# Optimization experiments

Measured on AMD Instinct MI355X. Metric: run time of the kernel, lower is better.

Reference implementation:

```python
import jax, jax.numpy as jnp
import numpy as np

B, L, D, H = 2, 2048, 1024, 16
DH = D // H


def setup_inputs() -> dict:
    key = jax.random.key(0)
    ks = jax.random.split(key, 12)
    s = 0.02
    return {
        "q": jax.random.normal(ks[0], (B, L, D), jnp.float32),
        "k": jax.random.normal(ks[1], (B, L, D), jnp.float32),
        "v": jax.random.normal(ks[2], (B, L, D), jnp.float32),
        "pos_enc": jax.random.normal(ks[3], (L + 1, D), jnp.float32),
        "Wq": jax.random.normal(ks[4], (D, D), jnp.float32) * s,
        "bq": jnp.zeros((D,), jnp.float32),
        "Wk": jax.random.normal(ks[5], (D, D), jnp.float32) * s,
        "bk": jnp.zeros((D,), jnp.float32),
        "Wv": jax.random.normal(ks[6], (D, D), jnp.float32) * s,
        "bv": jnp.zeros((D,), jnp.float32),
        "Wo": jax.random.normal(ks[7], (D, D), jnp.float32) * s,
        "bo": jnp.zeros((D,), jnp.float32),
        "r_w_bias": jax.random.normal(ks[8], (H, 1, DH), jnp.float32) * s,
        "r_r_bias": jax.random.normal(ks[9], (H, 1, DH), jnp.float32) * s,
        "r_kernel": jax.random.normal(ks[10], (H, D, DH), jnp.float32) * s,
    }


def reference(q, k, v, pos_enc, Wq, bq, Wk, bk, Wv, bv, Wo, bo,
              r_w_bias, r_r_bias, r_kernel):
    b, lq, d = q.shape
    h, _, dh = r_w_bias.shape
    lk = k.shape[1]
    scale = dh ** -0.5

    # q/k/v projections, then split heads: [b, l, d] -> [b, h, l, dh]
    qh = (q @ Wq + bq).reshape(b, lq, h, dh).transpose(0, 2, 1, 3)
    kh = (k @ Wk + bk).reshape(b, lk, h, dh).transpose(0, 2, 1, 3)
    vh = (v @ Wv + bv).reshape(b, lk, h, dh).transpose(0, 2, 1, 3)

    # content scores with global content bias (Transformer-XL r_w_bias)
    scores = jnp.einsum('bhqd,bhkd->bhqk', qh + r_w_bias, kh) * scale

    # relative-position term: pos_enc [p, d] @ r_kernel [h, d, dh] -> [h, p, dh]
    pe = jnp.einsum('pd,hde->hpe', pos_enc, r_kernel)
    rel = jnp.einsum('bhqd,hpd->bhqp', qh + r_r_bias, pe) * scale  # [b,h,lq,p]
    p = rel.shape[-1]
    shift = 1 + (lq != lk)
    # rel-shift trick: reshape with swapped last two dims, drop first `shift`
    # rows, reshape back, keep first lk columns
    rel = rel.reshape(b, h, p, lq)[:, :, shift:, :]
    rel = rel.reshape(b, h, lq, p - shift)[..., :lk]
    scores = scores + rel

    # causal mask (key_cache is None path): subtract 1e7 on strict upper triangle
    causal_mask = jnp.triu(jnp.ones((lq, lk), dtype=bool), 1)
    scores = scores - causal_mask * 1e7

    out = jnp.einsum('bhqk,bhkd->bhqd', jax.nn.softmax(scores, axis=-1), vh)
    out = out.transpose(0, 2, 1, 3).reshape(b, lq, d)  # merge heads
    return out @ Wo + bo
```

## Files before the change

### kernel.cpp

```cpp
#include <hip/hip_runtime.h>
#include <hip/hip_bf16.h>

typedef __attribute__((ext_vector_type(8))) short bf16x8;
typedef __attribute__((ext_vector_type(4))) float f32x4;
typedef __attribute__((ext_vector_type(16))) float f32x16;
typedef unsigned short u16;
typedef unsigned int u32;

#define DEV static __device__ __forceinline__

DEV u16 f2us(float x) {
  __hip_bfloat16 h = __float2bfloat16(x);
  union { __hip_bfloat16 h; u16 u; } c; c.h = h; return c.u;
}
DEV float us2f(u16 u) {
  union { __hip_bfloat16 h; u16 u; } c; c.u = u;
  return __bfloat162float(c.h);
}
DEV f32x16 mfma32(bf16x8 a, bf16x8 b, f32x16 c) {
  return __builtin_amdgcn_mfma_f32_32x32x16_bf16(a, b, c, 0, 0, 0);
}
DEV u32 pkbf(float a, float b) {
  return (u32)f2us(a) | ((u32)f2us(b) << 16);
}
DEV void gl16(const u16* g, u16* l) {
  __builtin_amdgcn_global_load_lds(
      (const __attribute__((address_space(1))) unsigned int*)(g),
      (__attribute__((address_space(3))) unsigned int*)(l), 16, 0, 0);
}

constexpr int PE_ROWS = 2144;
constexpr int PE_M    = 2176;
constexpr float QSCALE = 0.125f;

constexpr size_t SZ_QKV  = (size_t)4096 * 1024 * 2;
constexpr size_t SZ_W    = (size_t)1024 * 1024 * 2;
constexpr size_t SZ_POSB = (size_t)PE_M * 1024 * 2;
constexpr size_t OFF_QB   = 0;
constexpr size_t OFF_KB   = OFF_QB  + SZ_QKV;
constexpr size_t OFF_VB   = OFF_KB  + SZ_QKV;
constexpr size_t OFF_WQT  = OFF_VB  + SZ_QKV;
constexpr size_t OFF_WKT  = OFF_WQT + SZ_W;
constexpr size_t OFF_WVT  = OFF_WKT + SZ_W;
constexpr size_t OFF_WOT  = OFF_WVT + SZ_W;
constexpr size_t OFF_RKT  = OFF_WOT + SZ_W;
constexpr size_t OFF_POSB = OFF_RKT + SZ_W;
constexpr size_t OFF_QW   = OFF_POSB + SZ_POSB;
constexpr size_t OFF_QR   = OFF_QW  + SZ_QKV;
constexpr size_t OFF_KH   = OFF_QR  + SZ_QKV;
constexpr size_t OFF_VT   = OFF_KH  + SZ_QKV;
constexpr size_t OFF_PEH  = OFF_VT  + SZ_QKV;
constexpr size_t OFF_ATTNB = OFF_QB;

struct PrepPtrs {
  const float4 *q, *k, *v, *pos;
  u16 *qb, *kb, *vb, *posb;
  const float *Wq, *Wk, *Wv, *Wo, *rk;
  u16 *Wqt, *Wkt, *Wvt, *Wot, *Rkt;
};

__global__ __launch_bounds__(256)
void k_prep(PrepPtrs P)
{
  __shared__ float t[32][33];
  const int bid = blockIdx.x;
  if (bid < 14464) {
    const float4* src; u16* dst; int i, n4in, n4tot;
    if (bid < 4096)       { src = P.q;   dst = P.qb;   i = bid * 256 + threadIdx.x;           n4in = 1048576; n4tot = 1048576; }
    else if (bid < 8192)  { src = P.k;   dst = P.kb;   i = (bid - 4096) * 256 + threadIdx.x;  n4in = 1048576; n4tot = 1048576; }
    else if (bid < 12288) { src = P.v;   dst = P.vb;   i = (bid - 8192) * 256 + threadIdx.x;  n4in = 1048576; n4tot = 1048576; }
    else                  { src = P.pos; dst = P.posb; i = (bid - 12288) * 256 + threadIdx.x; n4in = 524544;  n4tot = 557056; }
    if (i >= n4tot) return;
    float4 val;
    if (i < n4in) val = src[i];
    else { val.x = val.y = val.z = val.w = 0.f; }
    ushort4 o;
    o.x = f2us(val.x); o.y = f2us(val.y); o.z = f2us(val.z); o.w = f2us(val.w);
    *reinterpret_cast<ushort4*>(dst + (size_t)i * 4) = o;
    return;
  }
  const int tx = threadIdx.x & 31, ty = threadIdx.x >> 5;
  if (bid < 18560) {
    const int tt = bid - 14464;
    const int z = tt >> 10, rr = tt & 1023;
    const float* in = (z == 0) ? P.Wq : (z == 1) ? P.Wk : (z == 2) ? P.Wv : P.Wo;
    u16* out = (z == 0) ? P.Wqt : (z == 1) ? P.Wkt : (z == 2) ? P.Wvt : P.Wot;
    const int kb0 = (rr & 31) * 32, nb0 = (rr >> 5) * 32;
#pragma unroll
    for (int r = 0; r < 32; r += 8)
      t[ty + r][tx] = in[(size_t)(kb0 + ty + r) * 1024 + nb0 + tx];
    __syncthreads();
#pragma unroll
    for (int r = 0; r < 32; r += 8)
      out[(size_t)(nb0 + ty + r) * 1024 + kb0 + tx] = f2us(t[tx][ty + r]);
    return;
  }
  {
    const int tt = bid - 18560;
    const int e = tt & 1, d = (tt >> 1) & 31, h = tt >> 6;
    const int eb0 = e * 32, db0 = d * 32;
#pragma unroll
    for (int r = 0; r < 32; r += 8)
      t[ty + r][tx] = P.rk[(size_t)h * 65536 + (size_t)(db0 + ty + r) * 64 + eb0 + tx];
    __syncthreads();
#pragma unroll
    for (int r = 0; r < 32; r += 8)
      P.Rkt[(size_t)(h * 64 + eb0 + ty + r) * 1024 + db0 + tx] = f2us(t[tx][ty + r]);
  }
}

struct ProjPtrs {
  const u16 *A0, *A1, *A2, *A3;
  const u16 *B0, *B1, *B2, *B3;
  const float *bias0, *bias1, *bias2;
  const float *rwb, *rrb;
  u16 *Qw, *Qr, *Kh, *Vt, *PEh;
};

__global__ __launch_bounds__(256)
void k_gemm_proj(ProjPtrs pp)
{
  const int z = blockIdx.z;
  if (z == 3 && blockIdx.y >= PE_M / 128) return;
  const u16* A  = (z == 0) ? pp.A0 : (z == 1) ? pp.A1 : (z == 2) ? pp.A2 : pp.A3;
  const u16* Bt = (z == 0) ? pp.B0 : (z == 1) ? pp.B1 : (z == 2) ? pp.B2 : pp.B3;

  __shared__ __attribute__((aligned(16))) u16 As[128 * 32];
  __shared__ __attribute__((aligned(16))) u16 Bs[128 * 32];
  const int tid  = threadIdx.x;
  const int lane = tid & 63;
  const int wave = tid >> 6;
  const int bm = blockIdx.y * 128;
  const int bn = blockIdx.x * 128;
  const int wr = (wave >> 1) * 64;
  const int wc = (wave & 1) * 64;
  const int fr = lane & 15;
  const int fk = (lane >> 4) * 8;

  f32x4 zero = {0.f, 0.f, 0.f, 0.f};
  f32x4 acc[4][4];
#pragma unroll
  for (int m = 0; m < 4; ++m)
#pragma unroll
    for (int n = 0; n < 4; ++n) acc[m][n] = zero;

  const int cA = wave * 2;
  const u16* gA = A  + (size_t)(bm + cA * 16 + (lane >> 2)) * 1024 + (lane & 3) * 8;
  const u16* gB = Bt + (size_t)(bn + cA * 16 + (lane >> 2)) * 1024 + (lane & 3) * 8;
  u16* lA = As + cA * 512;
  u16* lB = Bs + cA * 512;

  for (int k0 = 0; k0 < 1024; k0 += 32) {
    gl16(gA + k0, lA);
    gl16(gA + 16 * 1024 + k0, lA + 512);
    gl16(gB + k0, lB);
    gl16(gB + 16 * 1024 + k0, lB + 512);
    __syncthreads();
    bf16x8 af[4], bfv[4];
#pragma unroll
    for (int m = 0; m < 4; ++m) af[m]  = *(const bf16x8*)(&As[(wr + m * 16 + fr) * 32 + fk]);
#pragma unroll
    for (int n = 0; n < 4; ++n) bfv[n] = *(const bf16x8*)(&Bs[(wc + n * 16 + fr) * 32 + fk]);
#pragma unroll
    for (int m = 0; m < 4; ++m)
#pragma unroll
      for (int n = 0; n < 4; ++n)
        acc[m][n] = __builtin_amdgcn_mfma_f32_16x16x32_bf16(af[m], bfv[n], acc[m][n], 0, 0, 0);
    __syncthreads();
  }

#pragma unroll
  for (int m = 0; m < 4; ++m)
#pragma unroll
    for (int n = 0; n < 4; ++n)
#pragma unroll
      for (int r = 0; r < 4; ++r) {
        const int grow = bm + wr + m * 16 + (lane >> 4) * 4 + r;
        const int gcol = bn + wc + n * 16 + fr;
        float v = acc[m][n][r];
        const int b_ = grow >> 11, l_ = grow & 2047;
        const int h_ = gcol >> 6,  e_ = gcol & 63;
        if (z == 0) {
          v += pp.bias0[gcol];
          const size_t o = (((size_t)(b_ * 16 + h_) * 2048 + l_) << 6) + e_;
          pp.Qw[o] = f2us((v + pp.rwb[gcol]) * QSCALE);
          pp.Qr[o] = f2us((v + pp.rrb[gcol]) * QSCALE);
        } else if (z == 1) {
          v += pp.bias1[gcol];
          const size_t o = (((size_t)(b_ * 16 + h_) * 2048 + l_) << 6) + e_;
          pp.Kh[o] = f2us(v);
        } else if (z == 2) {
          v += pp.bias2[gcol];
          const size_t o = (((size_t)(b_ * 16 + h_) * 64 + e_) << 11) + l_;
          pp.Vt[o] = f2us(v);
        } else {
          if (grow < PE_ROWS) {
            const size_t o = ((size_t)h_ * PE_ROWS + grow) * 64 + e_;
            pp.PEh[o] = f2us(v);
          }
        }
      }
}

__global__ __launch_bounds__(256)
void k_gemm_o(const u16* __restrict__ A, const u16* __restrict__ Bt,
              const float* __restrict__ bias, float* __restrict__ outf)
{
  __shared__ __attribute__((aligned(16))) u16 As[128 * 32];
  __shared__ __attribute__((aligned(16))) u16 Bs[128 * 32];
  const int tid  = threadIdx.x;
  const int lane = tid & 63;
  const int wave = tid >> 6;
  const int bm = blockIdx.y * 128;
  const int bn = blockIdx.x * 128;
  const int wr = (wave >> 1) * 64;
  const int wc = (wave & 1) * 64;
  const int fr = lane & 15;
  const int fk = (lane >> 4) * 8;

  f32x4 zero = {0.f, 0.f, 0.f, 0.f};
  f32x4 acc[4][4];
#pragma unroll
  for (int m = 0; m < 4; ++m)
#pragma unroll
    for (int n = 0; n < 4; ++n) acc[m][n] = zero;

  const int cA = wave * 2;
  const u16* gA = A  + (size_t)(bm + cA * 16 + (lane >> 2)) * 1024 + (lane & 3) * 8;
  const u16* gB = Bt + (size_t)(bn + cA * 16 + (lane >> 2)) * 1024 + (lane & 3) * 8;
  u16* lA = As + cA * 512;
  u16* lB = Bs + cA * 512;

  for (int k0 = 0; k0 < 1024; k0 += 32) {
    gl16(gA + k0, lA);
    gl16(gA + 16 * 1024 + k0, lA + 512);
    gl16(gB + k0, lB);
    gl16(gB + 16 * 1024 + k0, lB + 512);
    __syncthreads();
    bf16x8 af[4], bfv[4];
#pragma unroll
    for (int m = 0; m < 4; ++m) af[m]  = *(const bf16x8*)(&As[(wr + m * 16 + fr) * 32 + fk]);
#pragma unroll
    for (int n = 0; n < 4; ++n) bfv[n] = *(const bf16x8*)(&Bs[(wc + n * 16 + fr) * 32 + fk]);
#pragma unroll
    for (int m = 0; m < 4; ++m)
#pragma unroll
      for (int n = 0; n < 4; ++n)
        acc[m][n] = __builtin_amdgcn_mfma_f32_16x16x32_bf16(af[m], bfv[n], acc[m][n], 0, 0, 0);
    __syncthreads();
  }

#pragma unroll
  for (int m = 0; m < 4; ++m)
#pragma unroll
    for (int n = 0; n < 4; ++n)
#pragma unroll
      for (int r = 0; r < 4; ++r) {
        const int grow = bm + wr + m * 16 + (lane >> 4) * 4 + r;
        const int gcol = bn + wc + n * 16 + fr;
        outf[(size_t)grow * 1024 + gcol] = acc[m][n][r] + bias[gcol];
      }
}


#define PV_HALF(WARR)                                                          \
  {                                                                            \
    _Pragma("unroll")                                                          \
    for (int kvs = 0; kvs < 2; ++kvs) {                                        \
      u32 snd0 = hi ? WARR[4 * kvs]     : WARR[4 * kvs + 2];                   \
      u32 snd1 = hi ? WARR[4 * kvs + 1] : WARR[4 * kvs + 3];                   \
      u32 r0 = (u32)__shfl_xor((int)snd0, 32);                                 \
      u32 r1 = (u32)__shfl_xor((int)snd1, 32);                                 \
      union { u32 u[4]; bf16x8 v; } pf;                                        \
      pf.u[0] = hi ? r0 : WARR[4 * kvs];                                       \
      pf.u[1] = hi ? r1 : WARR[4 * kvs + 1];                                   \
      pf.u[2] = hi ? WARR[4 * kvs + 2] : r0;                                   \
      pf.u[3] = hi ? WARR[4 * kvs + 3] : r1;                                   \
      bf16x8 v0_ = *(const bf16x8*)(V_h + (size_t)l31 * 2048 + c0h_            \
                                    + kvs * 16 + hi * 8);                      \
      bf16x8 v1_ = *(const bf16x8*)(V_h + (size_t)(32 + l31) * 2048 + c0h_     \
                                    + kvs * 16 + hi * 8);                      \
      Oc0 = mfma32(v0_, pf.v, Oc0);                                            \
      Oc1 = mfma32(v1_, pf.v, Oc1);                                            \
    }                                                                          \
  }

#define ATTN_HALF(q0v, c0_, KT)                                                \
  {                                                                            \
    const int c0h_ = (c0_) + (KT) * 32;                                        \
    f32x16 sv_ = {};                                                           \
    {                                                                          \
      bf16x8 qwf_[4], kf_[4];                                                  \
      _Pragma("unroll")                                                        \
      for (int kk = 0; kk < 4; ++kk) {                                         \
        qwf_[kk] = *(const bf16x8*)(Qw_h + (size_t)((q0v) + l31) * 64          \
                                    + kk * 16 + hi * 8);                       \
        kf_[kk] = *(const bf16x8*)(K_h + (size_t)(c0h_ + l31) * 64 + kk * 16   \
                                   + hi * 8);                                  \
      }                                                                        \
      _Pragma("unroll")                                                        \
      for (int kk = 0; kk < 4; ++kk) sv_ = mfma32(kf_[kk], qwf_[kk], sv_);     \
    }                                                                          \
    _Pragma("unroll")                                                          \
    for (int r = 0; r < 16; ++r) {                                             \
      const int pat = (r & 3) + 8 * (r >> 2) + 4 * hi;                         \
      float x = sv_[r] + us2f(Ew[l31][(KT) * 32 + pat + 31 - l31]);            \
      if (c0h_ + pat > (q0v) + l31) x = -1e30f;                                \
      sv_[r] = x;                                                              \
    }                                                                          \
    float mx_ = sv_[0];                                                        \
    _Pragma("unroll")                                                          \
    for (int r = 1; r < 16; ++r) mx_ = fmaxf(mx_, sv_[r]);                     \
    mx_ = fmaxf(mx_, __shfl_xor(mx_, 32));                                     \
    const float mn_ = fmaxf(mrun, mx_);                                        \
    const float al_ = __expf(mrun - mn_);                                      \
    mrun = mn_;                                                                \
    float rsum_ = 0.f;                                                         \
    u32 wa_[8];                                                                \
    _Pragma("unroll")                                                          \
    for (int g8 = 0; g8 < 8; ++g8) {                                           \
      float pa_ = __expf(sv_[2 * g8] - mn_);                                   \
      float pb_ = __expf(sv_[2 * g8 + 1] - mn_);                               \
      u16 ua_ = f2us(pa_), ub_ = f2us(pb_);                                    \
      rsum_ += us2f(ua_) + us2f(ub_);                                          \
      wa_[g8] = (u32)ua_ | ((u32)ub_ << 16);                                   \
    }                                                                          \
    ls = ls * al_ + rsum_ + __shfl_xor(rsum_, 32);                             \
    Oc0 *= al_;                                                                \
    Oc1 *= al_;                                                                \
    PV_HALF(wa_)                                                               \
  }

#define ATTN_STEP(q0v, stv)                                                    \
  {                                                                            \
    const int c0_ = (stv) * 64;                                                \
    const int Jb_ = 2048 + c0_ - (q0v) - 31;                                   \
    {                                                                          \
      bf16x8 qrf_[4];                                                          \
      _Pragma("unroll")                                                        \
      for (int kk = 0; kk < 4; ++kk)                                           \
        qrf_[kk] = *(const bf16x8*)(Qr_h + (size_t)((q0v) + l31) * 64          \
                                    + kk * 16 + hi * 8);                       \
      _Pragma("unroll")                                                        \
      for (int tau = 0; tau < 3; ++tau) {                                      \
        f32x16 e_ = {};                                                        \
        {                                                                      \
          bf16x8 pe_[4];                                                       \
          _Pragma("unroll")                                                    \
          for (int kk = 0; kk < 4; ++kk)                                       \
            pe_[kk] = *(const bf16x8*)(PE_h + (size_t)(Jb_ + tau * 32 + l31)   \
                                       * 64 + kk * 16 + hi * 8);               \
          _Pragma("unroll")                                                    \
          for (int kk = 0; kk < 4; ++kk) e_ = mfma32(pe_[kk], qrf_[kk], e_);   \
        }                                                                      \
        _Pragma("unroll")                                                      \
        for (int g4 = 0; g4 < 4; ++g4) {                                       \
          uint2 w2_;                                                           \
          w2_.x = pkbf(e_[4 * g4 + 0], e_[4 * g4 + 1]);                        \
          w2_.y = pkbf(e_[4 * g4 + 2], e_[4 * g4 + 3]);                        \
          *(uint2*)(&Ew[l31][tau * 32 + 8 * g4 + 4 * hi]) = w2_;               \
        }                                                                      \
      }                                                                        \
    }                                                                          \
    ATTN_HALF(q0v, c0_, 0)                                                     \
    ATTN_HALF(q0v, c0_, 1)                                                     \
  }

#define OBROUND(PRE, SCL)                                                      \
  {                                                                            \
    _Pragma("unroll")                                                          \
    for (int g4 = 0; g4 < 4; ++g4) {                                           \
      float* pb0 = &Obuf[l31][8 * g4 + 4 * hi];                                \
      float* pb1 = &Obuf[l31][32 + 8 * g4 + 4 * hi];                           \
      float2 a0 = *(float2*)pb0,       a1 = *(float2*)(pb0 + 2);               \
      float2 b0 = *(float2*)pb1,       b1 = *(float2*)(pb1 + 2);               \
      a0.x = a0.x * (PRE) + Oc0[4 * g4 + 0] * (SCL);                           \
      a0.y = a0.y * (PRE) + Oc0[4 * g4 + 1] * (SCL);                           \
      a1.x = a1.x * (PRE) + Oc0[4 * g4 + 2] * (SCL);                           \
      a1.y = a1.y * (PRE) + Oc0[4 * g4 + 3] * (SCL);                           \
      b0.x = b0.x * (PRE) + Oc1[4 * g4 + 0] * (SCL);                           \
      b0.y = b0.y * (PRE) + Oc1[4 * g4 + 1] * (SCL);                           \
      b1.x = b1.x * (PRE) + Oc1[4 * g4 + 2] * (SCL);                           \
      b1.y = b1.y * (PRE) + Oc1[4 * g4 + 3] * (SCL);                           \
      *(float2*)pb0 = a0; *(float2*)(pb0 + 2) = a1;                            \
      *(float2*)pb1 = b0; *(float2*)(pb1 + 2) = b1;                            \
    }                                                                          \
  }

__global__ __launch_bounds__(256, 4)
void k_attn(const u16* __restrict__ Qw, const u16* __restrict__ Qr,
            const u16* __restrict__ Kh, const u16* __restrict__ Vt,
            const u16* __restrict__ PEh, u16* __restrict__ attnb)
{
  const int bid = blockIdx.x;
  const int xcd = bid & 7, s = bid >> 3;
  const int p = s & 31, g = s >> 5;
  const int hb = xcd + 8 * g;
  const int h = hb & 15, b = hb >> 4;
  const int wave = threadIdx.x >> 6, lane = threadIdx.x & 63;
  const int l31 = lane & 31, hi = lane >> 5;

  const int qtL = 63 - p, qtS = p;
  const int q0L = qtL * 32, q0S = qtS * 32;
  const int nstL = qtL / 2 + 1;

  const u16* Qw_h = Qw + (size_t)hb * (2048 * 64);
  const u16* Qr_h = Qr + (size_t)hb * (2048 * 64);
  const u16* K_h  = Kh + (size_t)hb * (2048 * 64);
  const u16* V_h  = Vt + (size_t)hb * (64 * 2048);
  const u16* PE_h = PEh + (size_t)h * (PE_ROWS * 64);

  __shared__ __attribute__((aligned(16))) u16 Elds_all[4][32][100];
  __shared__ float Obuf[32][66];
  __shared__ float mlb[2][4][2][32];
  u16 (*Ew)[100] = Elds_all[wave];

  const int lo  = wave ? 9 + 8 * (wave - 1) : 0;
  const int hiE = lo + (wave ? 8 : 9);
  const int la0 = lo;
  const int la1 = hiE < nstL ? hiE : nstL;
  const int lb0 = lo > nstL ? lo : nstL;
  const int lb1 = hiE;
  const bool hasL = la1 > la0;
  const bool hasS = lb1 > lb0;
  const bool crossing = hasL && hasS;

  const f32x16 vzero = {};
  f32x16 Oc0 = {}, Oc1 = {};
  float mrun = -1e30f, ls = 0.f;

  if (hasL) {
    for (int st = la0; st < la1; ++st) ATTN_STEP(q0L, st)
  }
  if (crossing) {
    OBROUND(0.f, 1.f)
    if (hi == 0) { mlb[0][wave][0][l31] = mrun; mlb[0][wave][1][l31] = ls; }
    Oc0 = vzero; Oc1 = vzero; mrun = -1e30f; ls = 0.f;
  }
  if (hasS) {
    for (int st = lb0 - nstL; st < lb1 - nstL; ++st) ATTN_STEP(q0S, st)
  }

  if (hi == 0) {
    if (crossing) {
      mlb[1][wave][0][l31] = mrun; mlb[1][wave][1][l31] = ls;
    } else if (hasL) {
      mlb[0][wave][0][l31] = mrun;  mlb[0][wave][1][l31] = ls;
      mlb[1][wave][0][l31] = -1e30f; mlb[1][wave][1][l31] = 0.f;
    } else {
      mlb[1][wave][0][l31] = mrun;  mlb[1][wave][1][l31] = ls;
      mlb[0][wave][0][l31] = -1e30f; mlb[0][wave][1][l31] = 0.f;
    }
  }
  __syncthreads();

  const bool cwExists = (nstL != 17) && (nstL != 25);
  const int  cw = (nstL < 25) ? 2 : 3;

  const float mstL = fmaxf(fmaxf(mlb[0][0][0][l31], mlb[0][1][0][l31]),
                           fmaxf(mlb[0][2][0][l31], mlb[0][3][0][l31]));
  if (wave == 0) {
    const float preL = cwExists ? __expf(mlb[0][cw][0][l31] - mstL) : 0.f;
    const float scl = __expf(mrun - mstL);
    OBROUND(preL, scl)
  }
  __syncthreads();
  if (wave == 1) {
    const float scl = __expf(mrun - mstL);
    OBROUND(1.f, scl)
  }
  __syncthreads();
  if (wave == 2 && hasL && !crossing) {
    const float scl = __expf(mrun - mstL);
    OBROUND(1.f, scl)
  }
  __syncthreads();
  if (wave == 0) {
    float lst = 0.f;
#pragma unroll
    for (int w = 0; w < 4; ++w)
      lst += mlb[0][w][1][l31] * __expf(mlb[0][w][0][l31] - mstL);
    const float inv = 1.f / lst;
    const size_t orow = ((size_t)(b * 2048 + q0L + l31)) * 1024 + h * 64 + hi * 32;
#pragma unroll
    for (int j4 = 0; j4 < 32; j4 += 4) {
      float2 t0 = *(float2*)&Obuf[l31][hi * 32 + j4];
      float2 t1 = *(float2*)&Obuf[l31][hi * 32 + j4 + 2];
      ushort4 st;
      st.x = f2us(t0.x * inv); st.y = f2us(t0.y * inv);
      st.z = f2us(t1.x * inv); st.w = f2us(t1.y * inv);
      *(ushort4*)(attnb + orow + j4) = st;
    }
  }
  __syncthreads();

  const float mstS = fmaxf(mlb[1][2][0][l31], mlb[1][3][0][l31]);
  if (wave == 2 && hasS) {
    const float scl = __expf(mrun - mstS);
    OBROUND(0.f, scl)
  }
  __syncthreads();
  if (wave == 3) {
    const float scl = __expf(mrun - mstS);
    const float pre = (nstL < 25) ? 1.f : 0.f;
    OBROUND(pre, scl)
  }
  __syncthreads();
  if (wave == 1) {
    float lst = mlb[1][2][1][l31] * __expf(mlb[1][2][0][l31] - mstS)
              + mlb[1][3][1][l31] * __expf(mlb[1][3][0][l31] - mstS);
    const float inv = 1.f / lst;
    const size_t orow = ((size_t)(b * 2048 + q0S + l31)) * 1024 + h * 64 + hi * 32;
#pragma unroll
    for (int j4 = 0; j4 < 32; j4 += 4) {
      float2 t0 = *(float2*)&Obuf[l31][hi * 32 + j4];
      float2 t1 = *(float2*)&Obuf[l31][hi * 32 + j4 + 2];
      ushort4 st;
      st.x = f2us(t0.x * inv); st.y = f2us(t0.y * inv);
      st.z = f2us(t1.x * inv); st.w = f2us(t1.y * inv);
      *(ushort4*)(attnb + orow + j4) = st;
    }
  }
}

extern "C" void kernel_launch(void* const* d_in, const int* in_sizes, int n_in,
                              void* d_out, int out_size, void* d_ws, size_t ws_size,
                              hipStream_t stream)
{
  const float* q   = (const float*)d_in[0];
  const float* k   = (const float*)d_in[1];
  const float* v   = (const float*)d_in[2];
  const float* pos = (const float*)d_in[3];
  const float* Wq  = (const float*)d_in[4];
  const float* bq  = (const float*)d_in[5];
  const float* Wk  = (const float*)d_in[6];
  const float* bk  = (const float*)d_in[7];
  const float* Wv  = (const float*)d_in[8];
  const float* bv  = (const float*)d_in[9];
  const float* Wo  = (const float*)d_in[10];
  const float* bo  = (const float*)d_in[11];
  const float* rwb = (const float*)d_in[12];
  const float* rrb = (const float*)d_in[13];
  const float* rk  = (const float*)d_in[14];

  char* ws = (char*)d_ws;
  u16* qb    = (u16*)(ws + OFF_QB);
  u16* kb    = (u16*)(ws + OFF_KB);
  u16* vb    = (u16*)(ws + OFF_VB);
  u16* Wqt   = (u16*)(ws + OFF_WQT);
  u16* Wkt   = (u16*)(ws + OFF_WKT);
  u16* Wvt   = (u16*)(ws + OFF_WVT);
  u16* Wot   = (u16*)(ws + OFF_WOT);
  u16* Rkt   = (u16*)(ws + OFF_RKT);
  u16* posb  = (u16*)(ws + OFF_POSB);
  u16* Qw    = (u16*)(ws + OFF_QW);
  u16* Qr    = (u16*)(ws + OFF_QR);
  u16* Kh    = (u16*)(ws + OFF_KH);
  u16* Vt    = (u16*)(ws + OFF_VT);
  u16* PEh   = (u16*)(ws + OFF_PEH);
  u16* attnb = (u16*)(ws + OFF_ATTNB);
  float* outf = (float*)d_out;

  PrepPtrs P;
  P.q = (const float4*)q; P.k = (const float4*)k; P.v = (const float4*)v;
  P.pos = (const float4*)pos;
  P.qb = qb; P.kb = kb; P.vb = vb; P.posb = posb;
  P.Wq = Wq; P.Wk = Wk; P.Wv = Wv; P.Wo = Wo; P.rk = rk;
  P.Wqt = Wqt; P.Wkt = Wkt; P.Wvt = Wvt; P.Wot = Wot; P.Rkt = Rkt;
  k_prep<<<dim3(19584), 256, 0, stream>>>(P);

  ProjPtrs pp;
  pp.A0 = qb;  pp.A1 = kb;  pp.A2 = vb;  pp.A3 = posb;
  pp.B0 = Wqt; pp.B1 = Wkt; pp.B2 = Wvt; pp.B3 = Rkt;
  pp.bias0 = bq; pp.bias1 = bk; pp.bias2 = bv;
  pp.rwb = rwb; pp.rrb = rrb;
  pp.Qw = Qw; pp.Qr = Qr; pp.Kh = Kh; pp.Vt = Vt; pp.PEh = PEh;
  k_gemm_proj<<<dim3(8, 32, 4), 256, 0, stream>>>(pp);

  k_attn<<<dim3(1024), 256, 0, stream>>>(Qw, Qr, Kh, Vt, PEh, attnb);

  k_gemm_o<<<dim3(8, 32), 256, 0, stream>>>(attnb, Wot, bo, outf);
}
```

Measured before the change: 243.4 us.

## Share double-buffered K/V LDS tiles across four per-wave query tiles in attention

The attention kernel is restructured so each block handles four 32-row query tiles (one per wave, paired short/long for causal balance) over a shared key sweep. K and V tiles are staged into swizzled, double-buffered LDS, replacing per-wave direct global loads. The previous split-KV work sharing across waves, with its LDS merge and multiple barriers, is removed. Grid halves to 512 blocks and launch bounds drop to 2 blocks/SM, trading occupancy and per-step barriers (waves finishing early still sync) for K/V reuse.

Result: slower. 268.2 us (+10.2%).

```diff
diff --git a/kernel.cpp b/kernel.cpp
--- a/kernel.cpp
+++ b/kernel.cpp
@@ -263,7 +263,22 @@
 }
 
 
-#define PV_HALF(WARR)                                                          \
+#define STAGE(STV, BB)                                                         \
+  {                                                                            \
+    const int c0s_ = (STV) * 64;                                               \
+    _Pragma("unroll")                                                          \
+    for (int cc = 0; cc < 2; ++cc) {                                           \
+      const int Pu = cc * 256 + wave * 64 + lane;                              \
+      const int ru = Pu >> 3;                                                  \
+      const int cbu = (Pu & 7) ^ (ru & 7);                                     \
+      gl16(K_h + (size_t)(c0s_ + ru) * 64 + cbu * 8,                           \
+           &KS[BB][(cc * 256 + wave * 64) * 8]);                               \
+      gl16(V_h + (size_t)ru * 2048 + c0s_ + cbu * 8,                           \
+           &VS[BB][(cc * 256 + wave * 64) * 8]);                               \
+    }                                                                          \
+  }
+
+#define PV_HALF(WARR, KT, BB)                                                  \
   {                                                                            \
     _Pragma("unroll")                                                          \
     for (int kvs = 0; kvs < 2; ++kvs) {                                        \
@@ -276,27 +291,27 @@
       pf.u[1] = hi ? r1 : WARR[4 * kvs + 1];                                   \
       pf.u[2] = hi ? WARR[4 * kvs + 2] : r0;                                   \
       pf.u[3] = hi ? WARR[4 * kvs + 3] : r1;                                   \
-      bf16x8 v0_ = *(const bf16x8*)(V_h + (size_t)l31 * 2048 + c0h_            \
-                                    + kvs * 16 + hi * 8);                      \
-      bf16x8 v1_ = *(const bf16x8*)(V_h + (size_t)(32 + l31) * 2048 + c0h_     \
-                                    + kvs * 16 + hi * 8);                      \
+      const int cbv_ = ((KT) * 4 + kvs * 2 + hi) ^ (l31 & 7);                  \
+      bf16x8 v0_ = *(const bf16x8*)(&VS[BB][l31 * 64 + cbv_ * 8]);             \
+      bf16x8 v1_ = *(const bf16x8*)(&VS[BB][(32 + l31) * 64 + cbv_ * 8]);      \
       Oc0 = mfma32(v0_, pf.v, Oc0);                                            \
       Oc1 = mfma32(v1_, pf.v, Oc1);                                            \
     }                                                                          \
   }
 
-#define ATTN_HALF(q0v, c0_, KT)                                                \
+#define ATTN_HALF(c0_, KT, BB)                                                 \
   {                                                                            \
     const int c0h_ = (c0_) + (KT) * 32;                                        \
     f32x16 sv_ = {};                                                           \
     {                                                                          \
+      const int rk_ = (KT) * 32 + l31;                                         \
       bf16x8 qwf_[4], kf_[4];                                                  \
       _Pragma("unroll")                                                        \
       for (int kk = 0; kk < 4; ++kk) {                                         \
-        qwf_[kk] = *(const bf16x8*)(Qw_h + (size_t)((q0v) + l31) * 64          \
+        qwf_[kk] = *(const bf16x8*)(Qw_h + (size_t)(q0 + l31) * 64             \
                                     + kk * 16 + hi * 8);                       \
-        kf_[kk] = *(const bf16x8*)(K_h + (size_t)(c0h_ + l31) * 64 + kk * 16   \
-                                   + hi * 8);                                  \
+        const int cbk_ = (kk * 2 + hi) ^ (rk_ & 7);                            \
+        kf_[kk] = *(const bf16x8*)(&KS[BB][rk_ * 64 + cbk_ * 8]);              \
       }                                                                        \
       _Pragma("unroll")                                                        \
       for (int kk = 0; kk < 4; ++kk) sv_ = mfma32(kf_[kk], qwf_[kk], sv_);     \
@@ -305,7 +320,7 @@
     for (int r = 0; r < 16; ++r) {                                             \
       const int pat = (r & 3) + 8 * (r >> 2) + 4 * hi;                         \
       float x = sv_[r] + us2f(Ew[l31][(KT) * 32 + pat + 31 - l31]);            \
-      if (c0h_ + pat > (q0v) + l31) x = -1e30f;                                \
+      if (c0h_ + pat > q0 + l31) x = -1e30f;                                   \
       sv_[r] = x;                                                              \
     }                                                                          \
     float mx_ = sv_[0];                                                        \
@@ -328,18 +343,18 @@
     ls = ls * al_ + rsum_ + __shfl_xor(rsum_, 32);                             \
     Oc0 *= al_;                                                                \
     Oc1 *= al_;                                                                \
-    PV_HALF(wa_)                                                               \
-  }
-
-#define ATTN_STEP(q0v, stv)                                                    \
+    PV_HALF(wa_, KT, BB)                                                       \
+  }
+
+#define ATTN_STEP(stv, BB)                                                     \
   {                                                                            \
     const int c0_ = (stv) * 64;                                                \
-    const int Jb_ = 2048 + c0_ - (q0v) - 31;                                   \
+    const int Jb_ = 2048 + c0_ - q0 - 31;                                      \
     {                                                                          \
       bf16x8 qrf_[4];                                                          \
       _Pragma("unroll")                                                        \
       for (int kk = 0; kk < 4; ++kk)                                           \
-        qrf_[kk] = *(const bf16x8*)(Qr_h + (size_t)((q0v) + l31) * 64          \
+        qrf_[kk] = *(const bf16x8*)(Qr_h + (size_t)(q0 + l31) * 64             \
                                     + kk * 16 + hi * 8);                       \
       _Pragma("unroll")                                                        \
       for (int tau = 0; tau < 3; ++tau) {                                      \
@@ -362,47 +377,28 @@
         }                                                                      \
       }                                                                        \
     }                                                                          \
-    ATTN_HALF(q0v, c0_, 0)                                                     \
-    ATTN_HALF(q0v, c0_, 1)                                                     \
-  }
-
-#define OBROUND(PRE, SCL)                                                      \
-  {                                                                            \
-    _Pragma("unroll")                                                          \
-    for (int g4 = 0; g4 < 4; ++g4) {                                           \
-      float* pb0 = &Obuf[l31][8 * g4 + 4 * hi];                                \
-      float* pb1 = &Obuf[l31][32 + 8 * g4 + 4 * hi];                           \
-      float2 a0 = *(float2*)pb0,       a1 = *(float2*)(pb0 + 2);               \
-      float2 b0 = *(float2*)pb1,       b1 = *(float2*)(pb1 + 2);               \
-      a0.x = a0.x * (PRE) + Oc0[4 * g4 + 0] * (SCL);                           \
-      a0.y = a0.y * (PRE) + Oc0[4 * g4 + 1] * (SCL);                           \
-      a1.x = a1.x * (PRE) + Oc0[4 * g4 + 2] * (SCL);                           \
-      a1.y = a1.y * (PRE) + Oc0[4 * g4 + 3] * (SCL);                           \
-      b0.x = b0.x * (PRE) + Oc1[4 * g4 + 0] * (SCL);                           \
-      b0.y = b0.y * (PRE) + Oc1[4 * g4 + 1] * (SCL);                           \
-      b1.x = b1.x * (PRE) + Oc1[4 * g4 + 2] * (SCL);                           \
-      b1.y = b1.y * (PRE) + Oc1[4 * g4 + 3] * (SCL);                           \
-      *(float2*)pb0 = a0; *(float2*)(pb0 + 2) = a1;                            \
-      *(float2*)pb1 = b0; *(float2*)(pb1 + 2) = b1;                            \
-    }                                                                          \
-  }
-
-__global__ __launch_bounds__(256, 4)
+    ATTN_HALF(c0_, 0, BB)                                                      \
+    ATTN_HALF(c0_, 1, BB)                                                      \
+  }
+
+__global__ __launch_bounds__(256, 2)
 void k_attn(const u16* __restrict__ Qw, const u16* __restrict__ Qr,
             const u16* __restrict__ Kh, const u16* __restrict__ Vt,
             const u16* __restrict__ PEh, u16* __restrict__ attnb)
 {
   const int bid = blockIdx.x;
   const int xcd = bid & 7, s = bid >> 3;
-  const int p = s & 31, g = s >> 5;
+  const int j = s & 15, g = s >> 4;
   const int hb = xcd + 8 * g;
   const int h = hb & 15, b = hb >> 4;
   const int wave = threadIdx.x >> 6, lane = threadIdx.x & 63;
   const int l31 = lane & 31, hi = lane >> 5;
 
-  const int qtL = 63 - p, qtS = p;
-  const int q0L = qtL * 32, q0S = qtS * 32;
-  const int nstL = qtL / 2 + 1;
+  const int qt = (wave == 0) ? 2 * j : (wave == 1) ? 2 * j + 1
+               : (wave == 2) ? 62 - 2 * j : 63 - 2 * j;
+  const int q0 = qt * 32;
+  const int nst = qt / 2 + 1;
+  const int NST = 32 - j;
 
   const u16* Qw_h = Qw + (size_t)hb * (2048 * 64);
   const u16* Qr_h = Qr + (size_t)hb * (2048 * 64);
@@ -410,116 +406,42 @@
   const u16* V_h  = Vt + (size_t)hb * (64 * 2048);
   const u16* PE_h = PEh + (size_t)h * (PE_ROWS * 64);
 
+  __shared__ __attribute__((aligned(16))) u16 KS[2][4096];
+  __shared__ __attribute__((aligned(16))) u16 VS[2][4096];
   __shared__ __attribute__((aligned(16))) u16 Elds_all[4][32][100];
-  __shared__ float Obuf[32][66];
-  __shared__ float mlb[2][4][2][32];
   u16 (*Ew)[100] = Elds_all[wave];
 
-  const int lo  = wave ? 9 + 8 * (wave - 1) : 0;
-  const int hiE = lo + (wave ? 8 : 9);
-  const int la0 = lo;
-  const int la1 = hiE < nstL ? hiE : nstL;
-  const int lb0 = lo > nstL ? lo : nstL;
-  const int lb1 = hiE;
-  const bool hasL = la1 > la0;
-  const bool hasS = lb1 > lb0;
-  const bool crossing = hasL && hasS;
-
-  const f32x16 vzero = {};
   f32x16 Oc0 = {}, Oc1 = {};
   float mrun = -1e30f, ls = 0.f;
 
-  if (hasL) {
-    for (int st = la0; st < la1; ++st) ATTN_STEP(q0L, st)
-  }
-  if (crossing) {
-    OBROUND(0.f, 1.f)
-    if (hi == 0) { mlb[0][wave][0][l31] = mrun; mlb[0][wave][1][l31] = ls; }
-    Oc0 = vzero; Oc1 = vzero; mrun = -1e30f; ls = 0.f;
-  }
-  if (hasS) {
-    for (int st = lb0 - nstL; st < lb1 - nstL; ++st) ATTN_STEP(q0S, st)
-  }
-
-  if (hi == 0) {
-    if (crossing) {
-      mlb[1][wave][0][l31] = mrun; mlb[1][wave][1][l31] = ls;
-    } else if (hasL) {
-      mlb[0][wave][0][l31] = mrun;  mlb[0][wave][1][l31] = ls;
-      mlb[1][wave][0][l31] = -1e30f; mlb[1][wave][1][l31] = 0.f;
-    } else {
-      mlb[1][wave][0][l31] = mrun;  mlb[1][wave][1][l31] = ls;
-      mlb[0][wave][0][l31] = -1e30f; mlb[0][wave][1][l31] = 0.f;
-    }
-  }
+  STAGE(0, 0)
   __syncthreads();
 
-  const bool cwExists = (nstL != 17) && (nstL != 25);
-  const int  cw = (nstL < 25) ? 2 : 3;
-
-  const float mstL = fmaxf(fmaxf(mlb[0][0][0][l31], mlb[0][1][0][l31]),
-                           fmaxf(mlb[0][2][0][l31], mlb[0][3][0][l31]));
-  if (wave == 0) {
-    const float preL = cwExists ? __expf(mlb[0][cw][0][l31] - mstL) : 0.f;
-    const float scl = __expf(mrun - mstL);
-    OBROUND(preL, scl)
-  }
-  __syncthreads();
-  if (wave == 1) {
-    const float scl = __expf(mrun - mstL);
-    OBROUND(1.f, scl)
-  }
-  __syncthreads();
-  if (wave == 2 && hasL && !crossing) {
-    const float scl = __expf(mrun - mstL);
-    OBROUND(1.f, scl)
-  }
-  __syncthreads();
-  if (wave == 0) {
-    float lst = 0.f;
-#pragma unroll
-    for (int w = 0; w < 4; ++w)
-      lst += mlb[0][w][1][l31] * __expf(mlb[0][w][0][l31] - mstL);
-    const float inv = 1.f / lst;
-    const size_t orow = ((size_t)(b * 2048 + q0L + l31)) * 1024 + h * 64 + hi * 32;
-#pragma unroll
-    for (int j4 = 0; j4 < 32; j4 += 4) {
-      float2 t0 = *(float2*)&Obuf[l31][hi * 32 + j4];
-      float2 t1 = *(float2*)&Obuf[l31][hi * 32 + j4 + 2];
-      ushort4 st;
-      st.x = f2us(t0.x * inv); st.y = f2us(t0.y * inv);
-      st.z = f2us(t1.x * inv); st.w = f2us(t1.y * inv);
-      *(ushort4*)(attnb + orow + j4) = st;
-    }
-  }
-  __syncthreads();
-
-  const float mstS = fmaxf(mlb[1][2][0][l31], mlb[1][3][0][l31]);
-  if (wave == 2 && hasS) {
-    const float scl = __expf(mrun - mstS);
-    OBROUND(0.f, scl)
-  }
-  __syncthreads();
-  if (wave == 3) {
-    const float scl = __expf(mrun - mstS);
-    const float pre = (nstL < 25) ? 1.f : 0.f;
-    OBROUND(pre, scl)
-  }
-  __syncthreads();
-  if (wave == 1) {
-    float lst = mlb[1][2][1][l31] * __expf(mlb[1][2][0][l31] - mstS)
-              + mlb[1][3][1][l31] * __expf(mlb[1][3][0][l31] - mstS);
-    const float inv = 1.f / lst;
-    const size_t orow = ((size_t)(b * 2048 + q0S + l31)) * 1024 + h * 64 + hi * 32;
-#pragma unroll
-    for (int j4 = 0; j4 < 32; j4 += 4) {
-      float2 t0 = *(float2*)&Obuf[l31][hi * 32 + j4];
-      float2 t1 = *(float2*)&Obuf[l31][hi * 32 + j4 + 2];
-      ushort4 st;
-      st.x = f2us(t0.x * inv); st.y = f2us(t0.y * inv);
-      st.z = f2us(t1.x * inv); st.w = f2us(t1.y * inv);
-      *(ushort4*)(attnb + orow + j4) = st;
-    }
+  int bb = 0;
+  for (int st = 0; st < NST; ++st) {
+    if (st + 1 < NST) STAGE(st + 1, bb ^ 1)
+    if (st < nst) ATTN_STEP(st, bb)
+    __syncthreads();
+    bb ^= 1;
+  }
+
+  const float inv = 1.f / ls;
+  const size_t orow = ((size_t)(b * 2048 + q0 + l31)) * 1024 + h * 64;
+#pragma unroll
+  for (int g4 = 0; g4 < 4; ++g4) {
+    const int d = 8 * g4 + 4 * hi;
+    ushort4 s0;
+    s0.x = f2us(Oc0[4 * g4 + 0] * inv);
+    s0.y = f2us(Oc0[4 * g4 + 1] * inv);
+    s0.z = f2us(Oc0[4 * g4 + 2] * inv);
+    s0.w = f2us(Oc0[4 * g4 + 3] * inv);
+    *(ushort4*)(attnb + orow + d) = s0;
+    ushort4 s1;
+    s1.x = f2us(Oc1[4 * g4 + 0] * inv);
+    s1.y = f2us(Oc1[4 * g4 + 1] * inv);
+    s1.z = f2us(Oc1[4 * g4 + 2] * inv);
+    s1.w = f2us(Oc1[4 * g4 + 3] * inv);
+    *(ushort4*)(attnb + orow + 32 + d) = s1;
   }
 }
 
@@ -577,7 +499,7 @@
   pp.Qw = Qw; pp.Qr = Qr; pp.Kh = Kh; pp.Vt = Vt; pp.PEh = PEh;
   k_gemm_proj<<<dim3(8, 32, 4), 256, 0, stream>>>(pp);
 
-  k_attn<<<dim3(1024), 256, 0, stream>>>(Qw, Qr, Kh, Vt, PEh, attnb);
+  k_attn<<<dim3(512), 256, 0, stream>>>(Qw, Qr, Kh, Vt, PEh, attnb);
 
   k_gemm_o<<<dim3(8, 32), 256, 0, stream>>>(attnb, Wot, bo, outf);
 }
```
